# Kernel optimization log

Hardware: AMD Instinct MI355X
Metric: run time of the kernel (lower is better)

The kernel has to match this reference:

```python
import jax, jax.numpy as jnp
import numpy as np

D_MODEL = 512
N_HEADS = 8
HEAD_DIM = D_MODEL // N_HEADS
B, T = 128, 256


def setup_inputs() -> dict:
    key = jax.random.key(0)
    ks = jax.random.split(key, 5)
    s = 1.0 / np.sqrt(D_MODEL)
    return {
        "x": jax.random.normal(ks[0], (B, T, D_MODEL), dtype=jnp.float32),
        "W_qkv": jax.random.uniform(ks[1], (D_MODEL, 3 * D_MODEL), jnp.float32, -s, s),
        "b_qkv": jax.random.uniform(ks[2], (3 * D_MODEL,), jnp.float32, -s, s),
        "W_out": jax.random.uniform(ks[3], (D_MODEL, D_MODEL), jnp.float32, -s, s),
        "b_out": jax.random.uniform(ks[4], (D_MODEL,), jnp.float32, -s, s),
    }


def reference(x, W_qkv, b_qkv, W_out, b_out):
    Bsz, Tlen, C = x.shape
    H, hd = N_HEADS, HEAD_DIM
    qkv = x @ W_qkv + b_qkv                       # [B,T,3C]
    qkv = qkv.reshape(Bsz, Tlen, 3, H, hd).transpose(2, 0, 3, 1, 4)  # [3,B,H,T,hd]
    q, k, v = qkv[0], qkv[1], qkv[2]
    att = jnp.einsum('bhtd,bhsd->bhts', q, k) * (1.0 / np.sqrt(hd))  # [B,H,T,T]
    causal = jnp.tril(jnp.ones((Tlen, Tlen), dtype=bool))
    att = jnp.where(causal, att, -jnp.inf)
    att = jax.nn.softmax(att, axis=-1)
    y = jnp.einsum('bhts,bhsd->bhtd', att, v)     # [B,H,T,hd]
    y = y.transpose(0, 2, 1, 3).reshape(Bsz, Tlen, C)
    return y @ W_out + b_out
```

## Files before the change

kernel.cpp:

```cpp
#include <hip/hip_runtime.h>
#include <hip/hip_bf16.h>

typedef __attribute__((ext_vector_type(4))) float f32x4;
typedef __attribute__((ext_vector_type(8))) short s16x8;
typedef unsigned short u16;

__device__ __forceinline__ u16 f2bf(float f) {
    union { float f; unsigned int u; } a; a.f = f;
    unsigned int u = a.u;
    unsigned int lsb = (u >> 16) & 1u;
    u += 0x7fffu + lsb;
    return (u16)(u >> 16);
}

__device__ __forceinline__ void gll16(const u16* g, u16* l) {
    __builtin_amdgcn_global_load_lds(
        (const __attribute__((address_space(1))) unsigned int*)g,
        (__attribute__((address_space(3))) unsigned int*)l, 16, 0, 0);
}


__global__ void cvt_x_kernel(const float* __restrict__ x, u16* __restrict__ xb, int n4) {
    int i = blockIdx.x * 256 + threadIdx.x;
    if (i < n4) {
        float4 v = ((const float4*)x)[i];
        ushort4 o;
        o.x = f2bf(v.x); o.y = f2bf(v.y); o.z = f2bf(v.z); o.w = f2bf(v.w);
        ((ushort4*)xb)[i] = o;
    }
}

template<int KK, int NN>
__global__ void cvt_wT_kernel(const float* __restrict__ w, u16* __restrict__ wt) {
    int id = blockIdx.x * 256 + threadIdx.x;
    if (id < NN * (KK / 8)) {
        int n = id % NN, kg = id / NN;
        union { u16 h[8]; int4 v; } o;
#pragma unroll
        for (int e = 0; e < 8; ++e) o.h[e] = f2bf(w[(kg * 8 + e) * NN + n]);
        *(int4*)&wt[n * KK + kg * 8] = o.v;
    }
}


__global__ __launch_bounds__(256) void vtrans_kernel(u16* __restrict__ V) {
    __shared__ __align__(16) u16 Vl[256 * 68];
    const int tid = threadIdx.x;
    u16* base = V + ((size_t)blockIdx.x << 14);
#pragma unroll
    for (int k = 0; k < 8; ++k) {
        int g = tid + k * 256;
        int t = g >> 3, dp = g & 7;
        *(int4*)&Vl[t * 68 + dp * 8] = *(const int4*)&base[g * 8];
    }
    __syncthreads();
#pragma unroll
    for (int k = 0; k < 8; ++k) {
        int g = tid + k * 256;
        int tc = g >> 8, rem = g & 255, d = rem >> 2, p8 = rem & 3;
        int tb = tc * 32 + p8 * 8;
        union { u16 h[8]; int4 v; } o;
#pragma unroll
        for (int e = 0; e < 8; ++e) o.h[e] = Vl[(tb + e) * 68 + d];
        *(int4*)&base[g * 8] = o.v;
    }
}


template<int K>
__device__ __forceinline__ void stage256(const u16* __restrict__ A, const u16* __restrict__ Bt,
                                         int m0, int n0, int kt, u16* As, u16* Bs) {
    const int lane = threadIdx.x & 63, w = threadIdx.x >> 6;
    const int lr = lane >> 3;
    const int lg = lane & 7;
    const int sgA = lg ^ lr;
#pragma unroll
    for (int j = 0; j < 4; ++j) {
        const int blk = w * 4 + j;
        gll16(&A[(m0 + blk * 8 + lr) * K + kt + sgA * 8], &As[blk * 512]);
    }
#pragma unroll
    for (int j = 0; j < 4; ++j) {
        const int blk = w * 4 + j;
        const int sgB = lg ^ ((2 * j + (lr >> 2)) & 7);
        gll16(&Bt[(n0 + blk * 8 + lr) * K + kt + sgB * 8], &Bs[blk * 512]);
    }
}

template<int K>
__device__ __forceinline__ void gemm_tile256(const u16* __restrict__ A, const u16* __restrict__ Bt,
                                             int m0, int n0,
                                             u16* As0, u16* Bs0, u16* As1, u16* Bs1,
                                             f32x4 (&acc)[8][4]) {
    const int lane = threadIdx.x & 63, li = lane & 15, quad = lane >> 4;
    const int w = threadIdx.x >> 6;
    const int wr = w >> 2, wc = w & 3;
    const int sw = li & 7;
    constexpr int NKT = K / 64;

    stage256<K>(A, Bt, m0, n0, 0, As0, Bs0);

#pragma unroll
    for (int kt = 0; kt < NKT; ++kt) {
        u16* Asc = (kt & 1) ? As1 : As0;
        u16* Bsc = (kt & 1) ? Bs1 : Bs0;
        if (kt + 1 < NKT) {
            stage256<K>(A, Bt, m0, n0, (kt + 1) * 64,
                        (kt & 1) ? As0 : As1, (kt & 1) ? Bs0 : Bs1);
            asm volatile("s_waitcnt vmcnt(8)\n\ts_barrier" ::: "memory");
        } else {
            asm volatile("s_waitcnt vmcnt(0)\n\ts_barrier" ::: "memory");
        }
        __builtin_amdgcn_s_setprio(1);
#pragma unroll
        for (int kc = 0; kc < 2; ++kc) {
            s16x8 af[8], bf[4];
#pragma unroll
            for (int i = 0; i < 8; ++i)
                af[i] = *(const s16x8*)&Asc[(wr * 128 + i * 16 + li) * 64 + (((quad + kc * 4) ^ sw)) * 8];
#pragma unroll
            for (int j = 0; j < 4; ++j)
                bf[j] = *(const s16x8*)&Bsc[(wc * 64 + li * 4 + j) * 64 + (((quad + kc * 4) ^ sw)) * 8];
#pragma unroll
            for (int i = 0; i < 8; ++i)
#pragma unroll
                for (int j = 0; j < 4; ++j)
                    acc[i][j] = __builtin_amdgcn_mfma_f32_16x16x32_bf16(af[i], bf[j], acc[i][j], 0, 0, 0);
        }
        __builtin_amdgcn_s_setprio(0);
        if (kt + 1 < NKT)
            asm volatile("s_barrier" ::: "memory");
    }
}


__global__ __launch_bounds__(512, 2) void gemm_qkv_kernel(const u16* __restrict__ xb,
                                                          const u16* __restrict__ WqkvT,
                                                          const float* __restrict__ b_qkv,
                                                          u16* __restrict__ Qb, u16* __restrict__ Kb,
                                                          u16* __restrict__ Vtb) {
    __shared__ __align__(16) u16 As0[256 * 64];
    __shared__ __align__(16) u16 Bs0[256 * 64];
    __shared__ __align__(16) u16 As1[256 * 64];
    __shared__ __align__(16) u16 Bs1[256 * 64];
    f32x4 acc[8][4];
#pragma unroll
    for (int i = 0; i < 8; ++i)
#pragma unroll
        for (int j = 0; j < 4; ++j) acc[i][j] = {0.f, 0.f, 0.f, 0.f};

    const int id = blockIdx.x, xcd = id & 7, slot = id >> 3;
    const int mt = xcd * 16 + slot / 6, nt = slot % 6;
    const int m0 = mt * 256, n0 = nt * 256;
    gemm_tile256<512>(xb, WqkvT, m0, n0, As0, Bs0, As1, Bs1, acc);

    const int lane = threadIdx.x & 63, li = lane & 15, quad = lane >> 4;
    const int w = threadIdx.x >> 6, wr = w >> 2, wc = w & 3;
    const int c0 = n0 + wc * 64;
    const int which = c0 >> 9, hh = (c0 >> 6) & 7;
    float4 b4 = *(const float4*)&b_qkv[c0 + li * 4];

#pragma unroll
    for (int i = 0; i < 8; ++i)
#pragma unroll
        for (int r = 0; r < 4; ++r) {
            int row = m0 + wr * 128 + i * 16 + quad * 4 + r;
            int bb = row >> 8, tt = row & 255;
            int bh = (bb * 8 + hh) << 14;
            u16 v0 = f2bf(acc[i][0][r] + b4.x), v1 = f2bf(acc[i][1][r] + b4.y);
            u16 v2 = f2bf(acc[i][2][r] + b4.z), v3 = f2bf(acc[i][3][r] + b4.w);
            if (which == 0) {
                *(ushort4*)&Qb[bh + tt * 64 + li * 4] = (ushort4){v0, v1, v2, v3};
            } else if (which == 1) {
                *(ushort4*)&Kb[bh + tt * 64 + li * 4] = (ushort4){v0, v1, v2, v3};
            } else {
                *(ushort4*)&Vtb[bh + tt * 64 + li * 4] = (ushort4){v0, v1, v2, v3};
            }
        }
}


__global__ __launch_bounds__(512, 2) void gemm_out_kernel(const u16* __restrict__ Yb,
                                                          const u16* __restrict__ WoutT,
                                                          const float* __restrict__ b_out,
                                                          float* __restrict__ out) {
    __shared__ __align__(16) u16 As0[256 * 64];
    __shared__ __align__(16) u16 Bs0[256 * 64];
    __shared__ __align__(16) u16 As1[256 * 64];
    __shared__ __align__(16) u16 Bs1[256 * 64];
    f32x4 acc[8][4];
#pragma unroll
    for (int i = 0; i < 8; ++i)
#pragma unroll
        for (int j = 0; j < 4; ++j) acc[i][j] = {0.f, 0.f, 0.f, 0.f};

    const int id = blockIdx.x, xcd = id & 7, slot = id >> 3;
    const int mt = xcd * 16 + (slot >> 1), nt = slot & 1;
    const int m0 = mt * 256, n0 = nt * 256;
    gemm_tile256<512>(Yb, WoutT, m0, n0, As0, Bs0, As1, Bs1, acc);

    const int lane = threadIdx.x & 63, li = lane & 15, quad = lane >> 4;
    const int w = threadIdx.x >> 6, wr = w >> 2, wc = w & 3;
    const int c0 = n0 + wc * 64;
    float4 b4 = *(const float4*)&b_out[c0 + li * 4];

#pragma unroll
    for (int i = 0; i < 8; ++i)
#pragma unroll
        for (int r = 0; r < 4; ++r) {
            int row = m0 + wr * 128 + i * 16 + quad * 4 + r;
            float4 o;
            o.x = acc[i][0][r] + b4.x; o.y = acc[i][1][r] + b4.y;
            o.z = acc[i][2][r] + b4.z; o.w = acc[i][3][r] + b4.w;
            *(float4*)&out[row * 512 + c0 + li * 4] = o;
        }
}


__global__ __launch_bounds__(256, 2) void attn_kernel(const u16* __restrict__ Qb,
                                                      const u16* __restrict__ Kb,
                                                      const u16* __restrict__ Vtb,
                                                      u16* __restrict__ Yb) {
    __shared__ __align__(16) u16 Ks[256 * 64];
    __shared__ __align__(16) u16 pl[4 * 2 * 16 * 40];

    const int tid = threadIdx.x, wave = tid >> 6, lane = tid & 63, li = lane & 15, quad = lane >> 4;
    const int bhid = blockIdx.x;
    const int b = bhid >> 3, h = bhid & 7;
    const int bh = bhid << 14;

    s16x8 qf0 = *(const s16x8*)&Qb[bh + (wave * 16 + li) * 64 + quad * 8];
    s16x8 qf1 = *(const s16x8*)&Qb[bh + (wave * 16 + li) * 64 + 32 + quad * 8];

    {
        const int lr = lane >> 3;
        const int sg = (lane & 7) ^ lr;
#pragma unroll
        for (int j = 0; j < 8; ++j) {
            int blk = wave * 8 + j;
            gll16(&Kb[bh + (blk * 8 + lr) * 64 + sg * 8], &Ks[blk * 512]);
        }
    }
    __syncthreads();

    u16* plw = &pl[wave * 1280];

    for (int p = 0; p < 4; ++p) {
        const int qt = p * 4 + wave;
        const int qrb = qt * 16;
        const int nst = qt + 1;

        f32x4 sacc[16];
#pragma unroll
        for (int st = 0; st < 16; ++st) sacc[st] = {0.f, 0.f, 0.f, 0.f};
        const int sw = li & 7;
#pragma unroll
        for (int g = 0; g < 4; ++g) {
            if (g * 4 < nst) {
                s16x8 kf[4][2];
#pragma unroll
                for (int t = 0; t < 4; ++t) {
                    if (g * 4 + t < nst) {
                        int rb = ((g * 4 + t) * 16 + li) * 64;
                        kf[t][0] = *(const s16x8*)&Ks[rb + ((quad    ) ^ sw) * 8];
                        kf[t][1] = *(const s16x8*)&Ks[rb + ((quad + 4) ^ sw) * 8];
                    }
                }
#pragma unroll
                for (int t = 0; t < 4; ++t) {
                    if (g * 4 + t < nst) {
                        sacc[g*4+t] = __builtin_amdgcn_mfma_f32_16x16x32_bf16(qf0, kf[t][0], sacc[g*4+t], 0, 0, 0);
                        sacc[g*4+t] = __builtin_amdgcn_mfma_f32_16x16x32_bf16(qf1, kf[t][1], sacc[g*4+t], 0, 0, 0);
                    }
                }
            }
        }

        s16x8 nqf0 = qf0, nqf1 = qf1;
        if (p < 3) {
            int nqrb = ((p + 1) * 4 + wave) * 16;
            nqf0 = *(const s16x8*)&Qb[bh + (nqrb + li) * 64 + quad * 8];
            nqf1 = *(const s16x8*)&Qb[bh + (nqrb + li) * 64 + 32 + quad * 8];
        }

        float mx[4] = {-3e38f, -3e38f, -3e38f, -3e38f};
#pragma unroll
        for (int st = 0; st < 16; ++st) {
            if (st < nst) {
                int sg2 = st * 16 + li;
#pragma unroll
                for (int r = 0; r < 4; ++r) {
                    int tg = qrb + quad * 4 + r;
                    float v = (sg2 <= tg) ? sacc[st][r] * 0.125f : -3e38f;
                    sacc[st][r] = v;
                    mx[r] = fmaxf(mx[r], v);
                }
            }
        }
#pragma unroll
        for (int d = 1; d < 16; d <<= 1)
#pragma unroll
            for (int r = 0; r < 4; ++r) mx[r] = fmaxf(mx[r], __shfl_xor(mx[r], d, 64));

        const int ns32 = (nst + 1) >> 1;
        float l[4] = {0.f, 0.f, 0.f, 0.f};
        f32x4 oacc[4];
#pragma unroll
        for (int dt = 0; dt < 4; ++dt) oacc[dt] = {0.f, 0.f, 0.f, 0.f};

        s16x8 vf[2][4];
#pragma unroll
        for (int dt = 0; dt < 4; ++dt)
            vf[0][dt] = *(const s16x8*)&Vtb[bh + (li * 4 + dt) * 32 + quad * 8];

#pragma unroll
        for (int c = 0; c < 8; ++c) {
            if (c < ns32) {
                if (c + 1 < ns32) {
#pragma unroll
                    for (int dt = 0; dt < 4; ++dt)
                        vf[(c + 1) & 1][dt] = *(const s16x8*)&Vtb[bh + (c + 1) * 2048 + (li * 4 + dt) * 32 + quad * 8];
                }
                u16* pb = plw + (c & 1) * 640;
#pragma unroll
                for (int half = 0; half < 2; ++half) {
                    int st = c * 2 + half;
#pragma unroll
                    for (int r = 0; r < 4; ++r) {
                        float e = (st < nst) ? __expf(sacc[st][r] - mx[r]) : 0.f;
                        l[r] += e;
                        pb[(quad * 4 + r) * 40 + half * 16 + li] = f2bf(e);
                    }
                }
                s16x8 pf = *(const s16x8*)&pb[li * 40 + quad * 8];
#pragma unroll
                for (int dt = 0; dt < 4; ++dt)
                    oacc[dt] = __builtin_amdgcn_mfma_f32_16x16x32_bf16(pf, vf[c & 1][dt], oacc[dt], 0, 0, 0);
            }
        }

#pragma unroll
        for (int d = 1; d < 16; d <<= 1)
#pragma unroll
            for (int r = 0; r < 4; ++r) l[r] += __shfl_xor(l[r], d, 64);

#pragma unroll
        for (int r = 0; r < 4; ++r) {
            int tg = qrb + quad * 4 + r;
            float inv = 1.0f / l[r];
            ushort4 o;
            o.x = f2bf(oacc[0][r] * inv); o.y = f2bf(oacc[1][r] * inv);
            o.z = f2bf(oacc[2][r] * inv); o.w = f2bf(oacc[3][r] * inv);
            *(ushort4*)&Yb[(b * 256 + tg) * 512 + h * 64 + li * 4] = o;
        }

        qf0 = nqf0; qf1 = nqf1;
    }
}


extern "C" void kernel_launch(void* const* d_in, const int* in_sizes, int n_in,
                              void* d_out, int out_size, void* d_ws, size_t ws_size,
                              hipStream_t stream) {
    const float* x     = (const float*)d_in[0];
    const float* W_qkv = (const float*)d_in[1];
    const float* b_qkv = (const float*)d_in[2];
    const float* W_out = (const float*)d_in[3];
    const float* b_out = (const float*)d_in[4];
    float* out = (float*)d_out;

    char* ws = (char*)d_ws;
    u16* Qb    = (u16*)(ws);
    u16* Kb    = (u16*)(ws + 33554432);
    u16* Vtb   = (u16*)(ws + 67108864);
    u16* WqkvT = (u16*)(ws + 100663296);
    u16* WoutT = (u16*)(ws + 102236160);
    u16* xb    = (u16*)(ws + 102760448);
    u16* Yb    = xb;
    if (ws_size < (size_t)136314880) return;

    cvt_x_kernel<<<16384, 256, 0, stream>>>(x, xb, 4194304);
    cvt_wT_kernel<512, 1536><<<384, 256, 0, stream>>>(W_qkv, WqkvT);
    cvt_wT_kernel<512, 512><<<128, 256, 0, stream>>>(W_out, WoutT);
    gemm_qkv_kernel<<<768, 512, 0, stream>>>(xb, WqkvT, b_qkv, Qb, Kb, Vtb);
    vtrans_kernel<<<1024, 256, 0, stream>>>(Vtb);
    attn_kernel<<<1024, 256, 0, stream>>>(Qb, Kb, Vtb, Yb);
    gemm_out_kernel<<<256, 512, 0, stream>>>(Yb, WoutT, b_out, out);
}
```

Measured before the change: 276.3 us.

## Split GEMM k-tile into four sub-phases interleaving prefetch with MFMA

Restructures the double-buffered 256x256 GEMM main loop into four sub-phases per k-tile. Each phase loads half of the A or B fragments, issues a quarter of the next tile's global-to-LDS prefetch, then runs 16 MFMAs, in the style of a ping-pong schedule. The goal is to spread memory issue across compute and cut register pressure by holding 4 A fragments instead of 8. In exchange it adds more s_barriers per k-tile, waits on vmcnt(0) at every tile start, and drops the outer-loop unroll.

Result: no change. 275.9 us (-0.2%).

```diff
diff --git a/kernel.cpp b/kernel.cpp
--- a/kernel.cpp
+++ b/kernel.cpp
@@ -68,68 +68,120 @@
 
 
 template<int K>
-__device__ __forceinline__ void stage256(const u16* __restrict__ A, const u16* __restrict__ Bt,
-                                         int m0, int n0, int kt, u16* As, u16* Bs) {
+__device__ __forceinline__ void stageA_half(const u16* __restrict__ A, int m0, int half, int kt, u16* As) {
     const int lane = threadIdx.x & 63, w = threadIdx.x >> 6;
-    const int lr = lane >> 3;
-    const int lg = lane & 7;
+    const int lr = lane >> 3, lg = lane & 7;
     const int sgA = lg ^ lr;
 #pragma unroll
-    for (int j = 0; j < 4; ++j) {
-        const int blk = w * 4 + j;
-        gll16(&A[(m0 + blk * 8 + lr) * K + kt + sgA * 8], &As[blk * 512]);
-    }
-#pragma unroll
-    for (int j = 0; j < 4; ++j) {
-        const int blk = w * 4 + j;
-        const int sgB = lg ^ ((2 * j + (lr >> 2)) & 7);
-        gll16(&Bt[(n0 + blk * 8 + lr) * K + kt + sgB * 8], &Bs[blk * 512]);
+    for (int j = 0; j < 2; ++j) {
+        const int blk = w * 2 + j;
+        gll16(&A[(m0 + half * 128 + blk * 8 + lr) * K + kt + sgA * 8],
+              &As[half * 8192 + blk * 512]);
+    }
+}
+
+template<int K>
+__device__ __forceinline__ void stageB_half(const u16* __restrict__ Bt, int n0, int half, int kt, u16* Bs) {
+    const int lane = threadIdx.x & 63, w = threadIdx.x >> 6;
+    const int lr = lane >> 3, lg = lane & 7;
+#pragma unroll
+    for (int j = 0; j < 2; ++j) {
+        const int blk = w * 2 + j;
+        const int sgB = lg ^ ((4 * w + 2 * j + (lr >> 2)) & 7);
+        gll16(&Bt[(n0 + half * 128 + blk * 8 + lr) * K + kt + sgB * 8],
+              &Bs[half * 8192 + blk * 512]);
     }
 }
 
 template<int K>
 __device__ __forceinline__ void gemm_tile256(const u16* __restrict__ A, const u16* __restrict__ Bt,
-                                             int m0, int n0,
-                                             u16* As0, u16* Bs0, u16* As1, u16* Bs1,
-                                             f32x4 (&acc)[8][4]) {
+                                             int m0, int n0, u16* S, f32x4 (&acc)[8][4]) {
     const int lane = threadIdx.x & 63, li = lane & 15, quad = lane >> 4;
     const int w = threadIdx.x >> 6;
     const int wr = w >> 2, wc = w & 3;
     const int sw = li & 7;
     constexpr int NKT = K / 64;
 
-    stage256<K>(A, Bt, m0, n0, 0, As0, Bs0);
-
-#pragma unroll
+    u16* AS0 = S;            u16* BS0 = S + 16384;
+    u16* AS1 = S + 32768;    u16* BS1 = S + 49152;
+
+    stageA_half<K>(A, m0, 0, 0, AS0);
+    stageA_half<K>(A, m0, 1, 0, AS0);
+    stageB_half<K>(Bt, n0, 0, 0, BS0);
+    stageB_half<K>(Bt, n0, 1, 0, BS0);
+
     for (int kt = 0; kt < NKT; ++kt) {
-        u16* Asc = (kt & 1) ? As1 : As0;
-        u16* Bsc = (kt & 1) ? Bs1 : Bs0;
-        if (kt + 1 < NKT) {
-            stage256<K>(A, Bt, m0, n0, (kt + 1) * 64,
-                        (kt & 1) ? As0 : As1, (kt & 1) ? Bs0 : Bs1);
-            asm volatile("s_waitcnt vmcnt(8)\n\ts_barrier" ::: "memory");
-        } else {
-            asm volatile("s_waitcnt vmcnt(0)\n\ts_barrier" ::: "memory");
-        }
+        u16* Ac = (kt & 1) ? AS1 : AS0;
+        u16* Bc = (kt & 1) ? BS1 : BS0;
+        u16* An = (kt & 1) ? AS0 : AS1;
+        u16* Bn = (kt & 1) ? BS0 : BS1;
+        const bool pf = (kt + 1 < NKT);
+        const int kn = (kt + 1) * 64;
+
+        asm volatile("s_waitcnt vmcnt(0)\n\ts_barrier" ::: "memory");
+
+        s16x8 af[4], bf[4];
+
+#pragma unroll
+        for (int i = 0; i < 4; ++i)
+            af[i] = *(const s16x8*)&Ac[(wr * 128 + i * 16 + li) * 64 + (quad ^ sw) * 8];
+#pragma unroll
+        for (int j = 0; j < 4; ++j)
+            bf[j] = *(const s16x8*)&Bc[(wc * 64 + li * 4 + j) * 64 + (quad ^ sw) * 8];
+        if (pf) stageA_half<K>(A, m0, 0, kn, An);
+        asm volatile("s_barrier" ::: "memory");
         __builtin_amdgcn_s_setprio(1);
 #pragma unroll
-        for (int kc = 0; kc < 2; ++kc) {
-            s16x8 af[8], bf[4];
-#pragma unroll
-            for (int i = 0; i < 8; ++i)
-                af[i] = *(const s16x8*)&Asc[(wr * 128 + i * 16 + li) * 64 + (((quad + kc * 4) ^ sw)) * 8];
+        for (int i = 0; i < 4; ++i)
 #pragma unroll
             for (int j = 0; j < 4; ++j)
-                bf[j] = *(const s16x8*)&Bsc[(wc * 64 + li * 4 + j) * 64 + (((quad + kc * 4) ^ sw)) * 8];
-#pragma unroll
-            for (int i = 0; i < 8; ++i)
-#pragma unroll
-                for (int j = 0; j < 4; ++j)
-                    acc[i][j] = __builtin_amdgcn_mfma_f32_16x16x32_bf16(af[i], bf[j], acc[i][j], 0, 0, 0);
-        }
+                acc[i][j] = __builtin_amdgcn_mfma_f32_16x16x32_bf16(af[i], bf[j], acc[i][j], 0, 0, 0);
         __builtin_amdgcn_s_setprio(0);
-        if (kt + 1 < NKT)
-            asm volatile("s_barrier" ::: "memory");
+        asm volatile("s_barrier" ::: "memory");
+
+#pragma unroll
+        for (int i = 0; i < 4; ++i)
+            af[i] = *(const s16x8*)&Ac[(wr * 128 + (4 + i) * 16 + li) * 64 + (quad ^ sw) * 8];
+        if (pf) stageA_half<K>(A, m0, 1, kn, An);
+        asm volatile("s_barrier" ::: "memory");
+        __builtin_amdgcn_s_setprio(1);
+#pragma unroll
+        for (int i = 0; i < 4; ++i)
+#pragma unroll
+            for (int j = 0; j < 4; ++j)
+                acc[4 + i][j] = __builtin_amdgcn_mfma_f32_16x16x32_bf16(af[i], bf[j], acc[4 + i][j], 0, 0, 0);
+        __builtin_amdgcn_s_setprio(0);
+        asm volatile("s_barrier" ::: "memory");
+
+#pragma unroll
+        for (int i = 0; i < 4; ++i)
+            af[i] = *(const s16x8*)&Ac[(wr * 128 + i * 16 + li) * 64 + ((quad + 4) ^ sw) * 8];
+#pragma unroll
+        for (int j = 0; j < 4; ++j)
+            bf[j] = *(const s16x8*)&Bc[(wc * 64 + li * 4 + j) * 64 + ((quad + 4) ^ sw) * 8];
+        if (pf) stageB_half<K>(Bt, n0, 0, kn, Bn);
+        asm volatile("s_barrier" ::: "memory");
+        __builtin_amdgcn_s_setprio(1);
+#pragma unroll
+        for (int i = 0; i < 4; ++i)
+#pragma unroll
+            for (int j = 0; j < 4; ++j)
+                acc[i][j] = __builtin_amdgcn_mfma_f32_16x16x32_bf16(af[i], bf[j], acc[i][j], 0, 0, 0);
+        __builtin_amdgcn_s_setprio(0);
+        asm volatile("s_barrier" ::: "memory");
+
+#pragma unroll
+        for (int i = 0; i < 4; ++i)
+            af[i] = *(const s16x8*)&Ac[(wr * 128 + (4 + i) * 16 + li) * 64 + ((quad + 4) ^ sw) * 8];
+        if (pf) stageB_half<K>(Bt, n0, 1, kn, Bn);
+        asm volatile("s_barrier" ::: "memory");
+        __builtin_amdgcn_s_setprio(1);
+#pragma unroll
+        for (int i = 0; i < 4; ++i)
+#pragma unroll
+            for (int j = 0; j < 4; ++j)
+                acc[4 + i][j] = __builtin_amdgcn_mfma_f32_16x16x32_bf16(af[i], bf[j], acc[4 + i][j], 0, 0, 0);
+        __builtin_amdgcn_s_setprio(0);
     }
 }
 
@@ -139,10 +191,7 @@
                                                           const float* __restrict__ b_qkv,
                                                           u16* __restrict__ Qb, u16* __restrict__ Kb,
                                                           u16* __restrict__ Vtb) {
-    __shared__ __align__(16) u16 As0[256 * 64];
-    __shared__ __align__(16) u16 Bs0[256 * 64];
-    __shared__ __align__(16) u16 As1[256 * 64];
-    __shared__ __align__(16) u16 Bs1[256 * 64];
+    __shared__ __align__(16) u16 S[65536];
     f32x4 acc[8][4];
 #pragma unroll
     for (int i = 0; i < 8; ++i)
@@ -152,7 +201,7 @@
     const int id = blockIdx.x, xcd = id & 7, slot = id >> 3;
     const int mt = xcd * 16 + slot / 6, nt = slot % 6;
     const int m0 = mt * 256, n0 = nt * 256;
-    gemm_tile256<512>(xb, WqkvT, m0, n0, As0, Bs0, As1, Bs1, acc);
+    gemm_tile256<512>(xb, WqkvT, m0, n0, S, acc);
 
     const int lane = threadIdx.x & 63, li = lane & 15, quad = lane >> 4;
     const int w = threadIdx.x >> 6, wr = w >> 2, wc = w & 3;
@@ -184,10 +233,7 @@
                                                           const u16* __restrict__ WoutT,
                                                           const float* __restrict__ b_out,
                                                           float* __restrict__ out) {
-    __shared__ __align__(16) u16 As0[256 * 64];
-    __shared__ __align__(16) u16 Bs0[256 * 64];
-    __shared__ __align__(16) u16 As1[256 * 64];
-    __shared__ __align__(16) u16 Bs1[256 * 64];
+    __shared__ __align__(16) u16 S[65536];
     f32x4 acc[8][4];
 #pragma unroll
     for (int i = 0; i < 8; ++i)
@@ -197,7 +243,7 @@
     const int id = blockIdx.x, xcd = id & 7, slot = id >> 3;
     const int mt = xcd * 16 + (slot >> 1), nt = slot & 1;
     const int m0 = mt * 256, n0 = nt * 256;
-    gemm_tile256<512>(Yb, WoutT, m0, n0, As0, Bs0, As1, Bs1, acc);
+    gemm_tile256<512>(Yb, WoutT, m0, n0, S, acc);
 
     const int lane = threadIdx.x & 63, li = lane & 15, quad = lane >> 4;
     const int w = threadIdx.x >> 6, wr = w >> 2, wc = w & 3;
```
